# Kernel tuning notes

Hardware: AMD Instinct MI355X
Metric: run time of the kernel (lower is better)

## Reference

```python
import jax, jax.numpy as jnp
import numpy as np

B, N, C = 2, 1024, 256
HEADS, DH = 8, 32
INNER = HEADS * DH
L, P = 3, 9
FF = 512
DEPTH = 2
KNN_K = (16, 64)
SHAPES_NP = np.array([[128, 128], [64, 64], [32, 32]], np.int32)
LEN = int((SHAPES_NP[:, 0] * SHAPES_NP[:, 1]).sum())


def _ln(x, g, b, eps=1e-5):
    m = x.mean(-1, keepdims=True)
    v = ((x - m) ** 2).mean(-1, keepdims=True)
    return (x - m) * jax.lax.rsqrt(v + eps) * g + b


def _knn_gather(x, pos, k):
    # pos: [B,N,3]; self-KNN (includes self as nearest)
    sq = jnp.sum(pos ** 2, -1)
    d2 = sq[:, :, None] + sq[:, None, :] - 2.0 * jnp.einsum('bnd,bmd->bnm', pos, pos)
    _, idx = jax.lax.top_k(-d2, k)  # [B,N,k]
    return jax.vmap(lambda xb, ib: xb[ib])(x, idx)  # [B,N,k,C]


def _self_attn_knn(x, pos3d, Wq, Wkv, Wo, bo, k):
    Bq, Nq, _ = x.shape
    knn_x = _knn_gather(x, pos3d, k)
    q = (x @ Wq).reshape(Bq, Nq, HEADS, DH)
    kk, vv = jnp.split(knn_x @ Wkv, 2, -1)
    kk = kk.reshape(Bq, Nq, k, HEADS, DH)
    vv = vv.reshape(Bq, Nq, k, HEADS, DH)
    attn = jax.nn.softmax(jnp.einsum('bnhd,bnshd->bnhs', q, kk) * (DH ** -0.5), -1)
    out = jnp.einsum('bnhs,bnshd->bnhd', attn, vv).reshape(Bq, Nq, INNER)
    return out @ Wo + bo


def _bilinear(value_l, loc, Hl, Wl):
    # value_l: [B, Hl*Wl, HEADS, DH]; loc: [B,N,HEADS,P,2] normalized [0,1]
    # grid_sample(align_corners=False, padding_mode='zeros') semantics
    Bq, Nq, Hh, Pp, _ = loc.shape
    xf = loc[..., 0] * Wl - 0.5
    yf = loc[..., 1] * Hl - 0.5
    x0 = jnp.floor(xf)
    y0 = jnp.floor(yf)
    out = jnp.zeros((Bq, Nq, Hh, Pp, DH), value_l.dtype)
    for dy in (0.0, 1.0):
        for dx in (0.0, 1.0):
            ix, iy = x0 + dx, y0 + dy
            w = (1.0 - jnp.abs(xf - ix)) * (1.0 - jnp.abs(yf - iy))
            valid = (ix >= 0) & (ix <= Wl - 1) & (iy >= 0) & (iy <= Hl - 1)
            flat = (jnp.clip(iy, 0, Hl - 1) * Wl + jnp.clip(ix, 0, Wl - 1)).astype(jnp.int32)
            flat = flat.transpose(0, 1, 3, 2).reshape(Bq, Nq * Pp, Hh)
            idx = jnp.broadcast_to(flat[..., None], (Bq, Nq * Pp, Hh, DH))
            g = jnp.take_along_axis(value_l, idx, axis=1)
            g = g.reshape(Bq, Nq, Pp, Hh, DH).transpose(0, 1, 3, 2, 4)
            out = out + g * (w * valid)[..., None]
    return out


def _msdeform(q, ref, value_src, Wval, bval, Woff, boff, Waw, baw, Wo, bo):
    Bq, Nq, _ = q.shape
    value = (value_src @ Wval + bval).reshape(Bq, -1, HEADS, DH)
    off = (q @ Woff + boff).reshape(Bq, Nq, HEADS, L, P, 2)
    aw = jax.nn.softmax((q @ Waw + baw).reshape(Bq, Nq, HEADS, L * P), -1)
    aw = aw.reshape(Bq, Nq, HEADS, L, P)
    normalizer = jnp.asarray(SHAPES_NP[:, ::-1].copy(), jnp.float32)  # (W,H) per level
    loc = ref[:, :, None, :, None, :] + off / normalizer[None, None, None, :, None, :]
    out = jnp.zeros((Bq, Nq, HEADS, DH), q.dtype)
    start = 0
    for l in range(L):
        Hl, Wl = int(SHAPES_NP[l, 0]), int(SHAPES_NP[l, 1])
        v_l = value[:, start:start + Hl * Wl]
        samp = _bilinear(v_l, loc[:, :, :, l], Hl, Wl)  # [B,N,H,P,DH]
        out = out + jnp.einsum('bnhpd,bnhp->bnhd', samp, aw[:, :, :, l])
        start += Hl * Wl
    return out.reshape(Bq, Nq, INNER) @ Wo + bo


def _forward(x, src, center_pos, center_pos3d, W_pos, b_pos, ln1_g, ln1_b, ln2_g, ln2_b, ln3_g, ln3_b,
             Wq, Wkv, Wo_sa, bo_sa, Wval, bval, Woff, boff, Waw, baw, Wo_ca, bo_ca, W1, b1, W2, b2):
    cpe = center_pos[..., 0, :] @ W_pos + b_pos  # pos_embedding(center_pos[...,0,:])
    ref = center_pos  # [B,N,L,2]
    for i in range(DEPTH):
        h = _ln(x + cpe, ln1_g[i], ln1_b[i])
        x = x + _self_attn_knn(h, center_pos3d, Wq[i], Wkv[i], Wo_sa[i], bo_sa[i], KNN_K[i])
        q = _ln(x, ln2_g[i], ln2_b[i]) + cpe  # with_pos_embed(norm(x), query_pos)
        s = _ln(src, ln2_g[i], ln2_b[i])      # PreNorm applies same LN to src
        x = x + _msdeform(q, ref, s, Wval[i], bval[i], Woff[i], boff[i], Waw[i], baw[i], Wo_ca[i], bo_ca[i])
        hf = _ln(x, ln3_g[i], ln3_b[i])
        x = x + (jax.nn.gelu(hf @ W1[i] + b1[i], approximate=False) @ W2[i] + b2[i])
    return x


def setup_inputs():
    key = jax.random.key(0)
    ks = iter(jax.random.split(key, 64))
    rn = lambda shape, s=1.0: jax.random.normal(next(ks), shape, jnp.float32) * s
    w = 0.02
    starts = np.concatenate([[0], np.cumsum(SHAPES_NP[:, 0] * SHAPES_NP[:, 1])[:-1]]).astype(np.int32)
    return {
        'x': rn((B, N, C)),
        'src': rn((B, LEN, C)),
        'center_pos': jax.random.uniform(next(ks), (B, N, L, 2), jnp.float32),
        'center_pos3d': rn((B, N, 3)),
        'spatial_shapes': jnp.asarray(SHAPES_NP),
        'level_start_index': jnp.asarray(starts),
        'W_pos': rn((2, C), w), 'b_pos': jnp.zeros((C,), jnp.float32),
        'ln1_g': jnp.ones((DEPTH, C)), 'ln1_b': jnp.zeros((DEPTH, C)),
        'ln2_g': jnp.ones((DEPTH, C)), 'ln2_b': jnp.zeros((DEPTH, C)),
        'ln3_g': jnp.ones((DEPTH, C)), 'ln3_b': jnp.zeros((DEPTH, C)),
        'Wq': rn((DEPTH, C, INNER), w), 'Wkv': rn((DEPTH, C, 2 * INNER), w),
        'Wo_sa': rn((DEPTH, INNER, C), w), 'bo_sa': jnp.zeros((DEPTH, C)),
        'Wval': rn((DEPTH, C, INNER), w), 'bval': jnp.zeros((DEPTH, INNER)),
        'Woff': rn((DEPTH, C, HEADS * L * P * 2), w), 'boff': rn((DEPTH, HEADS * L * P * 2), w),
        'Waw': rn((DEPTH, C, HEADS * L * P), w), 'baw': jnp.zeros((DEPTH, HEADS * L * P)),
        'Wo_ca': rn((DEPTH, INNER, C), w), 'bo_ca': jnp.zeros((DEPTH, C)),
        'W1': rn((DEPTH, C, FF), w), 'b1': jnp.zeros((DEPTH, FF)),
        'W2': rn((DEPTH, FF, C), w), 'b2': jnp.zeros((DEPTH, C)),
    }


def reference(x, src, center_pos, center_pos3d, spatial_shapes, level_start_index, W_pos, b_pos,
              ln1_g, ln1_b, ln2_g, ln2_b, ln3_g, ln3_b, Wq, Wkv, Wo_sa, bo_sa,
              Wval, bval, Woff, boff, Waw, baw, Wo_ca, bo_ca, W1, b1, W2, b2):
    # spatial_shapes / level_start_index are fixed constants (SHAPES_NP) baked into the level loop.
    return _forward(x, src, center_pos, center_pos3d, W_pos, b_pos, ln1_g, ln1_b, ln2_g, ln2_b,
                    ln3_g, ln3_b, Wq, Wkv, Wo_sa, bo_sa, Wval, bval, Woff, boff, Waw, baw,
                    Wo_ca, bo_ca, W1, b1, W2, b2)
```

## Files before the change

kernel.cpp:

```cpp
#include <hip/hip_runtime.h>
#include <math.h>


#define DEV __device__ __forceinline__

typedef __attribute__((ext_vector_type(8))) short bf16x8;
typedef __attribute__((ext_vector_type(4))) float floatx4;

DEV float gelu_f(float v) { return 0.5f * v * (1.0f + erff(v * 0.7071067811865475f)); }

DEV unsigned short f2bf(float f) {
    unsigned u = __float_as_uint(f);
    return (unsigned short)((u + 0x7fffu + ((u >> 16) & 1u)) >> 16);
}
DEV float bf2f(unsigned short s) { return __uint_as_float((unsigned)s << 16); }

__global__ __launch_bounds__(256) void k_lnsrc(const float* __restrict__ x, unsigned short* __restrict__ out) {
    int wid = threadIdx.x >> 6, lane = threadIdx.x & 63;
    size_t row = (size_t)blockIdx.x * 4 + wid;
    float4 v = ((const float4*)(x + row * 256))[lane];
    float s = (v.x + v.y) + (v.z + v.w);
#pragma unroll
    for (int o = 32; o; o >>= 1) s += __shfl_xor(s, o);
    float mean = s * (1.0f / 256.0f);
    float dx = v.x - mean, dy = v.y - mean, dz = v.z - mean, dw = v.w - mean;
    float q = (dx * dx + dy * dy) + (dz * dz + dw * dw);
#pragma unroll
    for (int o = 32; o; o >>= 1) q += __shfl_xor(q, o);
    float rstd = 1.0f / sqrtf(q * (1.0f / 256.0f) + 1e-5f);
    ushort4 o4;
    o4.x = f2bf(dx * rstd);
    o4.y = f2bf(dy * rstd);
    o4.z = f2bf(dz * rstd);
    o4.w = f2bf(dw * rstd);
    ((ushort4*)(out + row * 256))[lane] = o4;
}

__global__ __launch_bounds__(256) void k_lnfused(const float* __restrict__ x, const float* pre, const float* post,
                                                 const float* __restrict__ g, const float* __restrict__ b,
                                                 unsigned short* __restrict__ out) {
    int wid = threadIdx.x >> 6, lane = threadIdx.x & 63;
    size_t row = (size_t)blockIdx.x * 4 + wid;
    float4 v = ((const float4*)(x + row * 256))[lane];
    if (pre) {
        float4 p = ((const float4*)(pre + row * 256))[lane];
        v.x += p.x; v.y += p.y; v.z += p.z; v.w += p.w;
    }
    float s = (v.x + v.y) + (v.z + v.w);
#pragma unroll
    for (int o = 32; o; o >>= 1) s += __shfl_xor(s, o);
    float mean = s * (1.0f / 256.0f);
    float dx = v.x - mean, dy = v.y - mean, dz = v.z - mean, dw = v.w - mean;
    float q = (dx * dx + dy * dy) + (dz * dz + dw * dw);
#pragma unroll
    for (int o = 32; o; o >>= 1) q += __shfl_xor(q, o);
    float rstd = 1.0f / sqrtf(q * (1.0f / 256.0f) + 1e-5f);
    float4 gg = ((const float4*)g)[lane], bb = ((const float4*)b)[lane];
    float4 o4;
    o4.x = dx * rstd * gg.x + bb.x;
    o4.y = dy * rstd * gg.y + bb.y;
    o4.z = dz * rstd * gg.z + bb.z;
    o4.w = dw * rstd * gg.w + bb.w;
    if (post) {
        float4 p = ((const float4*)(post + row * 256))[lane];
        o4.x += p.x; o4.y += p.y; o4.z += p.z; o4.w += p.w;
    }
    ushort4 u4;
    u4.x = f2bf(o4.x); u4.y = f2bf(o4.y); u4.z = f2bf(o4.z); u4.w = f2bf(o4.w);
    ((ushort4*)(out + row * 256))[lane] = u4;
}

__global__ __launch_bounds__(256) void k_pre(const float* __restrict__ cpos, const float* __restrict__ Wp,
                                             const float* __restrict__ bp, float* __restrict__ cpe,
                                             const float* __restrict__ ln2b, const float* __restrict__ Wval,
                                             const float* __restrict__ bval, float* __restrict__ bval2) {
    int bid = blockIdx.x, tid = threadIdx.x;
    if (bid < 2048) {
        float px = cpos[(size_t)bid * 6 + 0], py = cpos[(size_t)bid * 6 + 1];
        cpe[(size_t)bid * 256 + tid] = px * Wp[tid] + py * Wp[256 + tid] + bp[tid];
    } else {
        int idx = (bid - 2048) * 4 + (tid >> 6);
        int d = idx >> 8, n = idx & 255;
        int lane = tid & 63;
        const float* W = Wval + (size_t)d * 65536 + n;
        const float* lb = ln2b + d * 256;
        float s = 0.0f;
#pragma unroll
        for (int kk = 0; kk < 4; kk++) {
            int k = lane + kk * 64;
            s = fmaf(lb[k], W[(size_t)k * 256], s);
        }
#pragma unroll
        for (int o = 32; o; o >>= 1) s += __shfl_xor(s, o);
        if (lane == 0) bval2[idx] = s + bval[idx];
    }
}

__global__ __launch_bounds__(256) void k_knn2(const float* __restrict__ pos, int* __restrict__ k16,
                                              int* __restrict__ k64) {
    __shared__ float sp[3072];
    int b = blockIdx.x >> 8;
    int n0 = (blockIdx.x & 255) * 4;
    for (int t = threadIdx.x; t < 3072; t += 256) sp[t] = pos[(size_t)b * 3072 + t];
    __syncthreads();
    int wid = threadIdx.x >> 6, lane = threadIdx.x & 63;
    int n = n0 + wid;
    float qx = sp[n * 3], qy = sp[n * 3 + 1], qz = sp[n * 3 + 2];
    float sqn = (qx * qx + qy * qy) + qz * qz;
    unsigned du[16];
#pragma unroll
    for (int t = 0; t < 16; t++) {
        int m = t * 64 + lane;
        float mx = sp[m * 3], my = sp[m * 3 + 1], mz = sp[m * 3 + 2];
        float sqm = (mx * mx + my * my) + mz * mz;
        float dt = (qx * mx + qy * my) + qz * mz;
        float d2 = (sqn + sqm) - 2.0f * dt;
        unsigned u = __float_as_uint(d2);
        du[t] = (u & 0x80000000u) ? ~u : (u | 0x80000000u);
    }
    unsigned long long lmask = (1ull << lane) - 1ull;

    auto cnt_le = [&](unsigned p) {
        int c = 0;
#pragma unroll
        for (int t = 0; t < 16; t++) c += __popcll(__ballot(du[t] <= p));
        return c;
    };
    auto find_T = [&](int K) {
        unsigned lo = 0u, hi = 0xFFFFFFFFu;
        while (lo < hi) {
            unsigned mid = lo + ((hi - lo) >> 1);
            if (cnt_le(mid) >= K) hi = mid; else lo = mid + 1;
        }
        return hi;
    };
    auto emit = [&](int K, unsigned T, int* out) {
        int base = 0;
#pragma unroll
        for (int t = 0; t < 16; t++) {
            bool lt = du[t] < T;
            unsigned long long mk = __ballot(lt);
            if (lt) out[base + __popcll(mk & lmask)] = t * 64 + lane;
            base += __popcll(mk);
        }
        int need = K - base, eb = 0;
#pragma unroll
        for (int t = 0; t < 16; t++) {
            bool eq = du[t] == T;
            unsigned long long mk = __ballot(eq);
            if (eq) {
                int r = eb + __popcll(mk & lmask);
                if (r < need) out[base + r] = t * 64 + lane;
            }
            eb += __popcll(mk);
        }
    };
    unsigned T16 = find_T(16);
    emit(16, T16, k16 + ((size_t)b * 1024 + n) * 16);
    unsigned T64 = find_T(64);
    emit(64, T64, k64 + ((size_t)b * 1024 + n) * 64);
}

template <int KK>
__global__ __launch_bounds__(256) void k_attn(const unsigned short* __restrict__ hqkv,
                                              const int* __restrict__ kidx, unsigned short* __restrict__ out) {
    int bn = blockIdx.x;
    int b = bn >> 10;
    int tid = threadIdx.x;
    __shared__ float sq[256];
    __shared__ float sa[8][KK];
    __shared__ int si[KK];
    if (tid < KK) si[tid] = kidx[(size_t)bn * KK + tid];
    sq[tid] = bf2f(hqkv[(size_t)bn * 768 + tid]) * 0.17677669529663689f;
    __syncthreads();
    const unsigned short* kvb = hqkv + (size_t)b * 1024 * 768;
#pragma unroll
    for (int pair = tid; pair < 8 * KK; pair += 256) {
        int s = pair & (KK - 1);
        int h = pair / KK;
        const uint4* kr = (const uint4*)(kvb + (size_t)si[s] * 768 + 256 + h * 32);
        const float* q4 = &sq[h * 32];
        float a0 = 0.f, a1 = 0.f;
#pragma unroll
        for (int e = 0; e < 4; e++) {
            uint4 kv = kr[e];
            const unsigned w[4] = {kv.x, kv.y, kv.z, kv.w};
#pragma unroll
            for (int u = 0; u < 4; u++) {
                float lo = __uint_as_float(w[u] << 16);
                float hi = __uint_as_float(w[u] & 0xffff0000u);
                a0 = fmaf(lo, q4[e * 8 + u * 2], a0);
                a1 = fmaf(hi, q4[e * 8 + u * 2 + 1], a1);
            }
        }
        sa[h][s] = a0 + a1;
    }
    __syncthreads();
    int h = tid >> 5, d = tid & 31;
    float mx = -1e30f;
    for (int s = d; s < KK; s += 32) mx = fmaxf(mx, sa[h][s]);
#pragma unroll
    for (int o = 16; o; o >>= 1) mx = fmaxf(mx, __shfl_xor(mx, o, 32));
    float sum = 0.0f;
    for (int s = d; s < KK; s += 32) {
        float e = __expf(sa[h][s] - mx);
        sa[h][s] = e;
        sum += e;
    }
#pragma unroll
    for (int o = 16; o; o >>= 1) sum += __shfl_xor(sum, o, 32);
    float inv = 1.0f / sum;
    __syncthreads();
    float acc = 0.0f;
    for (int s = 0; s < KK; s++) {
        float vv = bf2f(kvb[(size_t)si[s] * 768 + 512 + tid]);
        acc += sa[h][s] * vv;
    }
    out[(size_t)bn * 256 + tid] = f2bf(acc * inv);
}

__global__ __launch_bounds__(256) void k_msdeform(const float* __restrict__ offaw, const float* __restrict__ cpos,
                                                  const unsigned short* __restrict__ value_d,
                                                  unsigned short* __restrict__ out) {
    int bn = blockIdx.x;
    int b = bn >> 10;
    int tid = threadIdx.x;
    __shared__ float aw[216];
    __shared__ uint2 meta[864];
    __shared__ float sacc[2][256];
    if (tid < 216) aw[tid] = offaw[(size_t)bn * 648 + 432 + tid];
    __syncthreads();
    if (tid < 8) {
        float mx = -1e30f;
        for (int p = 0; p < 27; p++) mx = fmaxf(mx, aw[tid * 27 + p]);
        float s = 0.0f;
        for (int p = 0; p < 27; p++) {
            float e = __expf(aw[tid * 27 + p] - mx);
            aw[tid * 27 + p] = e;
            s += e;
        }
        float inv = 1.0f / s;
        for (int p = 0; p < 27; p++) aw[tid * 27 + p] *= inv;
    }
    __syncthreads();
    if (tid < 216) {
        int h = tid / 27, lp = tid - h * 27;
        int l = lp / 9;
        const int dims[3] = {128, 64, 32};
        const int starts[3] = {0, 16384, 20480};
        int Wl = dims[l], st = starts[l];
        float rx = cpos[(size_t)bn * 6 + l * 2], ry = cpos[(size_t)bn * 6 + l * 2 + 1];
        float ox = offaw[(size_t)bn * 648 + h * 54 + lp * 2];
        float oy = offaw[(size_t)bn * 648 + h * 54 + lp * 2 + 1];
        float rw = 1.0f / (float)Wl;
        float xf = (rx + ox * rw) * (float)Wl - 0.5f;
        float yf = (ry + oy * rw) * (float)Wl - 0.5f;
        float x0 = floorf(xf), y0 = floorf(yf);
        float wgt = aw[tid];
#pragma unroll
        for (int c = 0; c < 4; c++) {
            float ix = x0 + (float)(c & 1), iy = y0 + (float)(c >> 1);
            float w = (1.0f - fabsf(xf - ix)) * (1.0f - fabsf(yf - iy));
            bool valid = (ix >= 0.0f) & (ix <= (float)(Wl - 1)) & (iy >= 0.0f) & (iy <= (float)(Wl - 1));
            uint2 m;
            if (valid && w != 0.0f) {
                m.x = __float_as_uint(w * wgt);
                m.y = (unsigned)((st + (int)iy * Wl + (int)ix) * 1024);
            } else {
                m.x = 0u;
                m.y = 0u;
            }
            meta[tid * 4 + c] = m;
        }
    }
    __syncthreads();
    int par = tid >> 7, h2 = (tid >> 4) & 7, d2 = tid & 15;
    const char* base = (const char*)(value_d + (size_t)b * 21504 * 512) + h2 * 64 + d2 * 4;
    const uint2* mp = &meta[h2 * 108 + par * 54];
    float a0 = 0.f, a1 = 0.f;
#pragma unroll
    for (int j = 0; j < 54; j++) {
        uint2 m = mp[j];
        unsigned v = *(const unsigned*)(base + m.y);
        float w = __uint_as_float(m.x);
        a0 = fmaf(w, __uint_as_float(v << 16), a0);
        a1 = fmaf(w, __uint_as_float(v & 0xffff0000u), a1);
    }
    int ch = h2 * 32 + d2 * 2;
    sacc[par][ch] = a0;
    sacc[par][ch + 1] = a1;
    __syncthreads();
    out[(size_t)bn * 256 + tid] = f2bf(sacc[0][tid] + sacc[1][tid]);
}

struct TJobs {
    const float* src[18];
    const float* gam[18];
    unsigned short* dst[18];
    int K[18];
    int N[18];
};
__global__ __launch_bounds__(256) void k_tw(TJobs j) {
    int job = blockIdx.z;
    int K = j.K[job], N = j.N[job];
    int nt = (N + 31) >> 5, kt = K >> 5;
    if ((int)blockIdx.x >= nt || (int)blockIdx.y >= kt) return;
    __shared__ float t[32][33];
    const float* W = j.src[job];
    const float* g = j.gam[job];
    unsigned short* Wt = j.dst[job];
    int x = threadIdx.x & 31, y = threadIdx.x >> 5;
    int n0 = blockIdx.x << 5, k0 = blockIdx.y << 5;
#pragma unroll
    for (int i = 0; i < 32; i += 8) {
        int n = n0 + x;
        t[y + i][x] = (n < N) ? W[(size_t)(k0 + y + i) * N + n] : 0.0f;
    }
    __syncthreads();
    float gv = g ? g[k0 + x] : 1.0f;
#pragma unroll
    for (int i = 0; i < 32; i += 8) {
        int n = n0 + y + i;
        if (n < N) Wt[(size_t)n * K + k0 + x] = f2bf(gv * t[x][y + i]);
    }
}

template <int BM, int BN, int WGM, int WGN, bool BIAS, bool BIAS2, bool GELUF, bool RES, bool OBF16>
__global__ __launch_bounds__(256) void k_mgemm(const unsigned short* __restrict__ A,
                                               const unsigned short* __restrict__ Bt,
                                               const float* __restrict__ bias, const float* __restrict__ bias2,
                                               int bsplit, const float* __restrict__ res, void* __restrict__ Cout,
                                               int M, int K, int Ncol) {
    constexpr int BK = 32;
    constexpr int WAVE_M = BM / WGM, WAVE_N = BN / WGN;
    constexpr int FM = WAVE_M / 16, FN = WAVE_N / 16;
    constexpr int BUN = BN / 64;
    constexpr int AUN = BM * 4;
    __shared__ __align__(16) short a_lds[4][BM][8];
    __shared__ __align__(16) short b_lds[4][BN][8];
    int tid = threadIdx.x;
    int am0 = blockIdx.y * BM, bn0 = blockIdx.x * BN;
    int ar = tid >> 2, akc = tid & 3;
    const unsigned short* Arow = A + (size_t)(am0 + (ar & (BM - 1))) * K + akc * 8;
    int4 aq;
    int4 bq[BUN];
    int nsteps = K / BK;

    auto load_tile = [&](int k0) {
        if (AUN == 256 || tid < AUN) aq = *(const int4*)(Arow + k0);
#pragma unroll
        for (int jj = 0; jj < BUN; jj++) {
            int u = tid + 256 * jj;
            int col = u >> 2, kc = u & 3;
            int gn = bn0 + col;
            if (gn < Ncol)
                bq[jj] = *(const int4*)(Bt + (size_t)gn * K + k0 + kc * 8);
            else
                bq[jj] = make_int4(0, 0, 0, 0);
        }
    };
    auto write_lds = [&]() {
        if (AUN == 256 || tid < AUN) *(int4*)(&a_lds[akc][ar ^ akc][0]) = aq;
#pragma unroll
        for (int jj = 0; jj < BUN; jj++) {
            int u = tid + 256 * jj;
            int col = u >> 2, kc = u & 3;
            *(int4*)(&b_lds[kc][col ^ kc][0]) = bq[jj];
        }
    };
    int lane = tid & 63, wid = tid >> 6;
    int wm = wid / WGN, wn = wid % WGN;
    int fr = lane & 15, fkc = lane >> 4;
    floatx4 acc[FM][FN] = {};

    load_tile(0);
    for (int t = 0; t < nsteps; ++t) {
        if (t) __syncthreads();
        write_lds();
        __syncthreads();
        if (t + 1 < nsteps) load_tile((t + 1) * BK);
        bf16x8 af[FM], bf[FN];
#pragma unroll
        for (int m = 0; m < FM; m++) af[m] = *(const bf16x8*)(&a_lds[fkc][(wm * WAVE_M + m * 16 + fr) ^ fkc][0]);
#pragma unroll
        for (int n = 0; n < FN; n++) bf[n] = *(const bf16x8*)(&b_lds[fkc][(wn * WAVE_N + n * 16 + fr) ^ fkc][0]);
#pragma unroll
        for (int m = 0; m < FM; m++)
#pragma unroll
            for (int n = 0; n < FN; n++)
                acc[m][n] = __builtin_amdgcn_mfma_f32_16x16x32_bf16(af[m], bf[n], acc[m][n], 0, 0, 0);
    }
    int r4 = lane >> 4;
#pragma unroll
    for (int m = 0; m < FM; m++) {
        int row = am0 + wm * WAVE_M + m * 16 + r4 * 4;
#pragma unroll
        for (int n = 0; n < FN; n++) {
            int col = bn0 + wn * WAVE_N + n * 16 + fr;
            if (col < Ncol) {
                float bsc = 0.0f;
                if (BIAS) bsc = (BIAS2 && col >= bsplit) ? bias2[col - bsplit] : bias[col];
#pragma unroll
                for (int r = 0; r < 4; r++) {
                    size_t off = (size_t)(row + r) * Ncol + col;
                    float v = acc[m][n][r] + bsc;
                    if (GELUF) v = gelu_f(v);
                    if (RES) v += res[off];
                    if (OBF16)
                        ((unsigned short*)Cout)[off] = f2bf(v);
                    else
                        ((float*)Cout)[off] = v;
                }
            }
        }
    }
}

extern "C" void kernel_launch(void* const* d_in, const int* in_sizes, int n_in, void* d_out, int out_size,
                              void* d_ws, size_t ws_size, hipStream_t stream) {
    const float* xin = (const float*)d_in[0];
    const float* src = (const float*)d_in[1];
    const float* cpos = (const float*)d_in[2];
    const float* pos3 = (const float*)d_in[3];
    const float* Wpos = (const float*)d_in[6];
    const float* bpos = (const float*)d_in[7];
    const float* ln1g = (const float*)d_in[8];
    const float* ln1b = (const float*)d_in[9];
    const float* ln2g = (const float*)d_in[10];
    const float* ln2b = (const float*)d_in[11];
    const float* ln3g = (const float*)d_in[12];
    const float* ln3b = (const float*)d_in[13];
    const float* Wq = (const float*)d_in[14];
    const float* Wkv = (const float*)d_in[15];
    const float* Wosa = (const float*)d_in[16];
    const float* bosa = (const float*)d_in[17];
    const float* Wval = (const float*)d_in[18];
    const float* bval = (const float*)d_in[19];
    const float* Woff = (const float*)d_in[20];
    const float* boff = (const float*)d_in[21];
    const float* Waw = (const float*)d_in[22];
    const float* baw = (const float*)d_in[23];
    const float* Woca = (const float*)d_in[24];
    const float* boca = (const float*)d_in[25];
    const float* W1 = (const float*)d_in[26];
    const float* b1f = (const float*)d_in[27];
    const float* W2 = (const float*)d_in[28];
    const float* b2f = (const float*)d_in[29];
    float* x = (float*)d_out;

    float* ws = (float*)d_ws;
    float* cpe = ws;
    float* offaw = cpe + 524288;
    float* bval2 = offaw + 1327104;
    unsigned short* hqkv16 = (unsigned short*)(bval2 + 512);
    unsigned short* lnout16 = hqkv16 + 1572864;
    unsigned short* attn16 = lnout16 + 524288;
    unsigned short* cab16 = attn16 + 524288;
    unsigned short* ffmid16 = cab16 + 524288;
    unsigned short* srcn16 = ffmid16 + 1048576;
    unsigned short* value16 = srcn16 + 11010048;
    int* kidx16 = (int*)(value16 + 22020096);
    int* kidx64 = kidx16 + 32768;
    unsigned short* wt = (unsigned short*)(kidx64 + 131072);

    const size_t WT_STRIDE = 755712;
    const size_t O_WQKV = 0, O_WOSA = 196608, O_WOFFAW = 262144, O_WOCA = 428032,
                 O_W1 = 493568, O_W2 = 624640;
    unsigned short* wtval = wt + 2 * WT_STRIDE;

    TJobs tj;
    for (int d = 0; d < 2; d++) {
        unsigned short* wd = wt + (size_t)d * WT_STRIDE;
        int tb = d * 9;
        tj.src[tb + 0] = Wq + (size_t)d * 65536;    tj.gam[tb + 0] = nullptr;      tj.dst[tb + 0] = wd + O_WQKV;            tj.K[tb + 0] = 256; tj.N[tb + 0] = 256;
        tj.src[tb + 1] = Wkv + (size_t)d * 131072;  tj.gam[tb + 1] = nullptr;      tj.dst[tb + 1] = wd + O_WQKV + 65536;    tj.K[tb + 1] = 256; tj.N[tb + 1] = 512;
        tj.src[tb + 2] = Wosa + (size_t)d * 65536;  tj.gam[tb + 2] = nullptr;      tj.dst[tb + 2] = wd + O_WOSA;            tj.K[tb + 2] = 256; tj.N[tb + 2] = 256;
        tj.src[tb + 3] = Woff + (size_t)d * 110592; tj.gam[tb + 3] = nullptr;      tj.dst[tb + 3] = wd + O_WOFFAW;          tj.K[tb + 3] = 256; tj.N[tb + 3] = 432;
        tj.src[tb + 4] = Waw + (size_t)d * 55296;   tj.gam[tb + 4] = nullptr;      tj.dst[tb + 4] = wd + O_WOFFAW + 110592; tj.K[tb + 4] = 256; tj.N[tb + 4] = 216;
        tj.src[tb + 5] = Woca + (size_t)d * 65536;  tj.gam[tb + 5] = nullptr;      tj.dst[tb + 5] = wd + O_WOCA;            tj.K[tb + 5] = 256; tj.N[tb + 5] = 256;
        tj.src[tb + 6] = W1 + (size_t)d * 131072;   tj.gam[tb + 6] = nullptr;      tj.dst[tb + 6] = wd + O_W1;              tj.K[tb + 6] = 256; tj.N[tb + 6] = 512;
        tj.src[tb + 7] = W2 + (size_t)d * 131072;   tj.gam[tb + 7] = nullptr;      tj.dst[tb + 7] = wd + O_W2;              tj.K[tb + 7] = 512; tj.N[tb + 7] = 256;
        tj.src[tb + 8] = Wval + (size_t)d * 65536;  tj.gam[tb + 8] = ln2g + d * 256; tj.dst[tb + 8] = wtval + (size_t)d * 65536; tj.K[tb + 8] = 256; tj.N[tb + 8] = 256;
    }
    k_tw<<<dim3(16, 16, 18), 256, 0, stream>>>(tj);
    k_pre<<<2176, 256, 0, stream>>>(cpos, Wpos, bpos, cpe, ln2b, Wval, bval, bval2);
    k_lnsrc<<<10752, 256, 0, stream>>>(src, srcn16);
    k_knn2<<<512, 256, 0, stream>>>(pos3, kidx16, kidx64);

    k_mgemm<64, 256, 1, 4, true, false, false, false, true><<<dim3(2, 672), 256, 0, stream>>>(
        srcn16, wtval, bval2, nullptr, 0, nullptr, value16, 43008, 256, 512);

    for (int i = 0; i < 2; i++) {
        unsigned short* wd = wt + (size_t)i * WT_STRIDE;
        const float* xc = (i == 0) ? xin : x;
        k_lnfused<<<512, 256, 0, stream>>>(xc, cpe, nullptr, ln1g + i * 256, ln1b + i * 256, lnout16);
        k_mgemm<64, 64, 2, 2, false, false, false, false, true><<<dim3(12, 32), 256, 0, stream>>>(
            lnout16, wd + O_WQKV, nullptr, nullptr, 0, nullptr, hqkv16, 2048, 256, 768);
        if (i == 0)
            k_attn<16><<<2048, 256, 0, stream>>>(hqkv16, kidx16, attn16);
        else
            k_attn<64><<<2048, 256, 0, stream>>>(hqkv16, kidx64, attn16);
        k_mgemm<32, 64, 2, 2, true, false, false, true, false><<<dim3(4, 64), 256, 0, stream>>>(
            attn16, wd + O_WOSA, bosa + i * 256, nullptr, 0, xc, x, 2048, 256, 256);

        k_lnfused<<<512, 256, 0, stream>>>(x, nullptr, cpe, ln2g + i * 256, ln2b + i * 256, lnout16);
        k_mgemm<64, 64, 2, 2, true, true, false, false, false><<<dim3(11, 32), 256, 0, stream>>>(
            lnout16, wd + O_WOFFAW, boff + i * 432, baw + i * 216, 432, nullptr, offaw, 2048, 256, 648);
        k_msdeform<<<2048, 256, 0, stream>>>(offaw, cpos, value16 + (size_t)i * 256, cab16);
        k_mgemm<32, 64, 2, 2, true, false, false, true, false><<<dim3(4, 64), 256, 0, stream>>>(
            cab16, wd + O_WOCA, boca + i * 256, nullptr, 0, x, x, 2048, 256, 256);

        k_lnfused<<<512, 256, 0, stream>>>(x, nullptr, nullptr, ln3g + i * 256, ln3b + i * 256, lnout16);
        k_mgemm<64, 64, 2, 2, true, false, true, false, true><<<dim3(8, 32), 256, 0, stream>>>(
            lnout16, wd + O_W1, b1f + i * 512, nullptr, 0, nullptr, ffmid16, 2048, 256, 512);
        k_mgemm<32, 64, 2, 2, true, false, false, true, false><<<dim3(4, 64), 256, 0, stream>>>(
            ffmid16, wd + O_W2, b2f + i * 256, nullptr, 0, x, x, 2048, 512, 256);
    }
}
```

Baseline: 218.4 us.

## Fuse LayerNorm application into GEMM A-tile loads using precomputed row stats

Replaces the LayerNorm kernels that wrote a bf16 normalized buffer with a small row-statistics kernel (mean, rstd) plus a new GEMM variant that reads fp32 activations, applies the normalization, gamma/beta and optional pre/post add while staging A tiles into LDS. This removes the write and re-read of the intermediate normalized bf16 tensor. In exchange each GEMM column block re-reads fp32 A (twice the bytes of bf16) and redoes the normalization arithmetic, and a separate stats launch remains.

```diff
diff --git a/kernel.cpp b/kernel.cpp
--- a/kernel.cpp
+++ b/kernel.cpp
@@ -36,9 +36,8 @@
     ((ushort4*)(out + row * 256))[lane] = o4;
 }
 
-__global__ __launch_bounds__(256) void k_lnfused(const float* __restrict__ x, const float* pre, const float* post,
-                                                 const float* __restrict__ g, const float* __restrict__ b,
-                                                 unsigned short* __restrict__ out) {
+__global__ __launch_bounds__(256) void k_rowstats(const float* __restrict__ x, const float* pre,
+                                                  float* __restrict__ st) {
     int wid = threadIdx.x >> 6, lane = threadIdx.x & 63;
     size_t row = (size_t)blockIdx.x * 4 + wid;
     float4 v = ((const float4*)(x + row * 256))[lane];
@@ -54,20 +53,10 @@
     float q = (dx * dx + dy * dy) + (dz * dz + dw * dw);
 #pragma unroll
     for (int o = 32; o; o >>= 1) q += __shfl_xor(q, o);
-    float rstd = 1.0f / sqrtf(q * (1.0f / 256.0f) + 1e-5f);
-    float4 gg = ((const float4*)g)[lane], bb = ((const float4*)b)[lane];
-    float4 o4;
-    o4.x = dx * rstd * gg.x + bb.x;
-    o4.y = dy * rstd * gg.y + bb.y;
-    o4.z = dz * rstd * gg.z + bb.z;
-    o4.w = dw * rstd * gg.w + bb.w;
-    if (post) {
-        float4 p = ((const float4*)(post + row * 256))[lane];
-        o4.x += p.x; o4.y += p.y; o4.z += p.z; o4.w += p.w;
-    }
-    ushort4 u4;
-    u4.x = f2bf(o4.x); u4.y = f2bf(o4.y); u4.z = f2bf(o4.z); u4.w = f2bf(o4.w);
-    ((ushort4*)(out + row * 256))[lane] = u4;
+    if (lane == 0) {
+        st[row * 2] = mean;
+        st[row * 2 + 1] = 1.0f / sqrtf(q * (1.0f / 256.0f) + 1e-5f);
+    }
 }
 
 __global__ __launch_bounds__(256) void k_pre(const float* __restrict__ cpos, const float* __restrict__ Wp,
@@ -406,6 +395,122 @@
                     float v = acc[m][n][r] + bsc;
                     if (GELUF) v = gelu_f(v);
                     if (RES) v += res[off];
+                    if (OBF16)
+                        ((unsigned short*)Cout)[off] = f2bf(v);
+                    else
+                        ((float*)Cout)[off] = v;
+                }
+            }
+        }
+    }
+}
+
+template <int BN, bool PRE, bool POST, bool BIAS, bool BIAS2, bool GELUF, bool OBF16>
+__global__ __launch_bounds__(256) void k_lgemm(const float* __restrict__ A, const float* __restrict__ A2,
+                                               const float* __restrict__ stats, const float* __restrict__ lng,
+                                               const float* __restrict__ lnb,
+                                               const unsigned short* __restrict__ Bt,
+                                               const float* __restrict__ bias, const float* __restrict__ bias2,
+                                               int bsplit, void* __restrict__ Cout, int M, int K, int Ncol) {
+    constexpr int BM = 64, BK = 32;
+    constexpr int WGM = 2, WGN = 2;
+    constexpr int WAVE_M = BM / WGM, WAVE_N = BN / WGN;
+    constexpr int FM = WAVE_M / 16, FN = WAVE_N / 16;
+    constexpr int BUN = BN / 64;
+    __shared__ __align__(16) short a_lds[4][BM][8];
+    __shared__ __align__(16) short b_lds[4][BN][8];
+    int tid = threadIdx.x;
+    int am0 = blockIdx.y * BM, bn0 = blockIdx.x * BN;
+    int ar = tid >> 2, akc = tid & 3;
+    const float* Arow = A + (size_t)(am0 + ar) * K + akc * 8;
+    const float* A2row = (PRE || POST) ? (A2 + (size_t)(am0 + ar) * 256 + akc * 8) : nullptr;
+    float mean = stats[(size_t)(am0 + ar) * 2];
+    float rstd = stats[(size_t)(am0 + ar) * 2 + 1];
+    float4 a0, a1, p0, p1, g0, g1, c0, c1;
+    int4 bq[BUN];
+    int nsteps = K / BK;
+
+    auto load_tile = [&](int k0) {
+        a0 = *(const float4*)(Arow + k0);
+        a1 = *(const float4*)(Arow + k0 + 4);
+        if (PRE || POST) {
+            p0 = *(const float4*)(A2row + k0);
+            p1 = *(const float4*)(A2row + k0 + 4);
+        }
+        g0 = *(const float4*)(lng + k0 + akc * 8);
+        g1 = *(const float4*)(lng + k0 + akc * 8 + 4);
+        c0 = *(const float4*)(lnb + k0 + akc * 8);
+        c1 = *(const float4*)(lnb + k0 + akc * 8 + 4);
+#pragma unroll
+        for (int jj = 0; jj < BUN; jj++) {
+            int u = tid + 256 * jj;
+            int col = u >> 2, kc = u & 3;
+            int gn = bn0 + col;
+            if (gn < Ncol)
+                bq[jj] = *(const int4*)(Bt + (size_t)gn * K + k0 + kc * 8);
+            else
+                bq[jj] = make_int4(0, 0, 0, 0);
+        }
+    };
+    auto write_lds = [&]() {
+        float v[8] = {a0.x, a0.y, a0.z, a0.w, a1.x, a1.y, a1.z, a1.w};
+        float pp[8] = {p0.x, p0.y, p0.z, p0.w, p1.x, p1.y, p1.z, p1.w};
+        float gg[8] = {g0.x, g0.y, g0.z, g0.w, g1.x, g1.y, g1.z, g1.w};
+        float bb[8] = {c0.x, c0.y, c0.z, c0.w, c1.x, c1.y, c1.z, c1.w};
+        bf16x8 pk;
+#pragma unroll
+        for (int e = 0; e < 8; e++) {
+            float t = PRE ? (v[e] + pp[e]) : v[e];
+            float dx = t - mean;
+            float o = dx * rstd * gg[e] + bb[e];
+            if (POST) o += pp[e];
+            pk[e] = (short)f2bf(o);
+        }
+        *(bf16x8*)(&a_lds[akc][ar ^ akc][0]) = pk;
+#pragma unroll
+        for (int jj = 0; jj < BUN; jj++) {
+            int u = tid + 256 * jj;
+            int col = u >> 2, kc = u & 3;
+            *(int4*)(&b_lds[kc][col ^ kc][0]) = bq[jj];
+        }
+    };
+    int lane = tid & 63, wid = tid >> 6;
+    int wm = wid / WGN, wn = wid % WGN;
+    int fr = lane & 15, fkc = lane >> 4;
+    floatx4 acc[FM][FN] = {};
+
+    load_tile(0);
+    for (int t = 0; t < nsteps; ++t) {
+        if (t) __syncthreads();
+        write_lds();
+        __syncthreads();
+        if (t + 1 < nsteps) load_tile((t + 1) * BK);
+        bf16x8 af[FM], bf[FN];
+#pragma unroll
+        for (int m = 0; m < FM; m++) af[m] = *(const bf16x8*)(&a_lds[fkc][(wm * WAVE_M + m * 16 + fr) ^ fkc][0]);
+#pragma unroll
+        for (int n = 0; n < FN; n++) bf[n] = *(const bf16x8*)(&b_lds[fkc][(wn * WAVE_N + n * 16 + fr) ^ fkc][0]);
+#pragma unroll
+        for (int m = 0; m < FM; m++)
+#pragma unroll
+            for (int n = 0; n < FN; n++)
+                acc[m][n] = __builtin_amdgcn_mfma_f32_16x16x32_bf16(af[m], bf[n], acc[m][n], 0, 0, 0);
+    }
+    int r4 = lane >> 4;
+#pragma unroll
+    for (int m = 0; m < FM; m++) {
+        int row = am0 + wm * WAVE_M + m * 16 + r4 * 4;
+#pragma unroll
+        for (int n = 0; n < FN; n++) {
+            int col = bn0 + wn * WAVE_N + n * 16 + fr;
+            if (col < Ncol) {
+                float bsc = 0.0f;
+                if (BIAS) bsc = (BIAS2 && col >= bsplit) ? bias2[col - bsplit] : bias[col];
+#pragma unroll
+                for (int r = 0; r < 4; r++) {
+                    size_t off = (size_t)(row + r) * Ncol + col;
+                    float v = acc[m][n][r] + bsc;
+                    if (GELUF) v = gelu_f(v);
                     if (OBF16)
                         ((unsigned short*)Cout)[off] = f2bf(v);
                     else
@@ -452,9 +557,9 @@
     float* cpe = ws;
     float* offaw = cpe + 524288;
     float* bval2 = offaw + 1327104;
-    unsigned short* hqkv16 = (unsigned short*)(bval2 + 512);
-    unsigned short* lnout16 = hqkv16 + 1572864;
-    unsigned short* attn16 = lnout16 + 524288;
+    float* xstats = bval2 + 512;
+    unsigned short* hqkv16 = (unsigned short*)(xstats + 4096);
+    unsigned short* attn16 = hqkv16 + 1572864;
     unsigned short* cab16 = attn16 + 524288;
     unsigned short* ffmid16 = cab16 + 524288;
     unsigned short* srcn16 = ffmid16 + 1048576;
@@ -493,9 +598,9 @@
     for (int i = 0; i < 2; i++) {
         unsigned short* wd = wt + (size_t)i * WT_STRIDE;
         const float* xc = (i == 0) ? xin : x;
-        k_lnfused<<<512, 256, 0, stream>>>(xc, cpe, nullptr, ln1g + i * 256, ln1b + i * 256, lnout16);
-        k_mgemm<64, 64, 2, 2, false, false, false, false, true><<<dim3(12, 32), 256, 0, stream>>>(
-            lnout16, wd + O_WQKV, nullptr, nullptr, 0, nullptr, hqkv16, 2048, 256, 768);
+        k_rowstats<<<512, 256, 0, stream>>>(xc, cpe, xstats);
+        k_lgemm<64, true, false, false, false, false, true><<<dim3(12, 32), 256, 0, stream>>>(
+            xc, cpe, xstats, ln1g + i * 256, ln1b + i * 256, wd + O_WQKV, nullptr, nullptr, 0, hqkv16, 2048, 256, 768);
         if (i == 0)
             k_attn<16><<<2048, 256, 0, stream>>>(hqkv16, kidx16, attn16);
         else
@@ -503,16 +608,18 @@
         k_mgemm<32, 64, 2, 2, true, false, false, true, false><<<dim3(4, 64), 256, 0, stream>>>(
             attn16, wd + O_WOSA, bosa + i * 256, nullptr, 0, xc, x, 2048, 256, 256);
 
-        k_lnfused<<<512, 256, 0, stream>>>(x, nullptr, cpe, ln2g + i * 256, ln2b + i * 256, lnout16);
-        k_mgemm<64, 64, 2, 2, true, true, false, false, false><<<dim3(11, 32), 256, 0, stream>>>(
-            lnout16, wd + O_WOFFAW, boff + i * 432, baw + i * 216, 432, nullptr, offaw, 2048, 256, 648);
+        k_rowstats<<<512, 256, 0, stream>>>(x, nullptr, xstats);
+        k_lgemm<64, false, true, true, true, false, false><<<dim3(11, 32), 256, 0, stream>>>(
+            x, cpe, xstats, ln2g + i * 256, ln2b + i * 256, wd + O_WOFFAW, boff + i * 432, baw + i * 216, 432,
+            offaw, 2048, 256, 648);
         k_msdeform<<<2048, 256, 0, stream>>>(offaw, cpos, value16 + (size_t)i * 256, cab16);
         k_mgemm<32, 64, 2, 2, true, false, false, true, false><<<dim3(4, 64), 256, 0, stream>>>(
             cab16, wd + O_WOCA, boca + i * 256, nullptr, 0, x, x, 2048, 256, 256);
 
-        k_lnfused<<<512, 256, 0, stream>>>(x, nullptr, nullptr, ln3g + i * 256, ln3b + i * 256, lnout16);
-        k_mgemm<64, 64, 2, 2, true, false, true, false, true><<<dim3(8, 32), 256, 0, stream>>>(
-            lnout16, wd + O_W1, b1f + i * 512, nullptr, 0, nullptr, ffmid16, 2048, 256, 512);
+        k_rowstats<<<512, 256, 0, stream>>>(x, nullptr, xstats);
+        k_lgemm<64, false, false, true, false, true, true><<<dim3(8, 32), 256, 0, stream>>>(
+            x, nullptr, xstats, ln3g + i * 256, ln3b + i * 256, wd + O_W1, b1f + i * 512, nullptr, 0,
+            ffmid16, 2048, 256, 512);
         k_mgemm<32, 64, 2, 2, true, false, false, true, false><<<dim3(4, 64), 256, 0, stream>>>(
             ffmid16, wd + O_W2, b2f + i * 256, nullptr, 0, x, x, 2048, 512, 256);
     }
```

After: 238.2 us. 9.1% more time.
